# Performance work log

Measured on AMD Instinct MI355X. Metric: run time of the kernel, lower is better.

## Reference

```python
import jax, jax.numpy as jnp
import numpy as np

EC = 256   # ec
CT = 512   # ct
NH = 8     # heads
K = 3      # adaptive pool output
HC = EC // NH
CH = (256, 512, 1024)
HW = (48, 24, 12)
BS = 32
NT = 512   # number of text queries


def _ln(x, g, b, eps=1e-5):
    m = jnp.mean(x, axis=-1, keepdims=True)
    v = jnp.mean((x - m) ** 2, axis=-1, keepdims=True)
    return (x - m) * jax.lax.rsqrt(v + eps) * g + b


def _adaptive_max_pool(x, k):
    # H, W divisible by k -> uniform bins, identical to AdaptiveMaxPool2d
    B, C, H, W = x.shape
    return x.reshape(B, C, k, H // k, k, W // k).max(axis=(3, 5))


def setup_inputs() -> dict:
    key = jax.random.key(0)
    ks = jax.random.split(key, 32)
    d = {}
    for i, (c, s) in enumerate(zip(CH, HW)):
        d[f"x{i}"] = jax.random.normal(ks[i], (BS, c, s, s), jnp.float32)
    d["text"] = jax.random.normal(ks[3], (BS, NT, CT), jnp.float32)
    # 1x1 conv projections (stored as [C_in, EC] matrices)
    for i, c in enumerate(CH):
        d[f"w{i}"] = jax.random.normal(ks[4 + i], (c, EC), jnp.float32) / np.sqrt(c).astype(np.float32)
        d[f"cb{i}"] = jax.random.normal(ks[7 + i], (EC,), jnp.float32) * 0.02
    # LayerNorm + Linear for query (ct->ec), key/value (ec->ec)
    d["q_ln_g"] = jnp.ones((CT,), jnp.float32); d["q_ln_b"] = jnp.zeros((CT,), jnp.float32)
    d["k_ln_g"] = jnp.ones((EC,), jnp.float32); d["k_ln_b"] = jnp.zeros((EC,), jnp.float32)
    d["v_ln_g"] = jnp.ones((EC,), jnp.float32); d["v_ln_b"] = jnp.zeros((EC,), jnp.float32)
    d["q_w"] = jax.random.normal(ks[10], (CT, EC), jnp.float32) / np.sqrt(CT).astype(np.float32)
    d["q_b"] = jax.random.normal(ks[11], (EC,), jnp.float32) * 0.02
    d["k_w"] = jax.random.normal(ks[12], (EC, EC), jnp.float32) / np.sqrt(EC).astype(np.float32)
    d["k_b"] = jax.random.normal(ks[13], (EC,), jnp.float32) * 0.02
    d["v_w"] = jax.random.normal(ks[14], (EC, EC), jnp.float32) / np.sqrt(EC).astype(np.float32)
    d["v_b"] = jax.random.normal(ks[15], (EC,), jnp.float32) * 0.02
    d["proj_w"] = jax.random.normal(ks[16], (EC, CT), jnp.float32) / np.sqrt(EC).astype(np.float32)
    d["proj_b"] = jax.random.normal(ks[17], (CT,), jnp.float32) * 0.02
    return d


def reference(x0, x1, x2, text, w0, cb0, w1, cb1, w2, cb2,
              q_ln_g, q_ln_b, k_ln_g, k_ln_b, v_ln_g, v_ln_b,
              q_w, q_b, k_w, k_b, v_w, v_b, proj_w, proj_b):
    bs = x0.shape[0]
    feats = []
    for x, w, b in ((x0, w0, cb0), (x1, w1, cb1), (x2, w2, cb2)):
        p = jnp.einsum('bchw,ce->behw', x, w) + b[None, :, None, None]  # 1x1 conv
        feats.append(_adaptive_max_pool(p, K).reshape(bs, EC, K * K))
    xc = jnp.concatenate(feats, axis=-1).transpose(0, 2, 1)  # (bs, 27, ec)

    q = _ln(text, q_ln_g, q_ln_b) @ q_w + q_b   # (bs, NT, ec)
    k = _ln(xc, k_ln_g, k_ln_b) @ k_w + k_b     # (bs, 27, ec)
    v = _ln(xc, v_ln_g, v_ln_b) @ v_w + v_b     # (bs, 27, ec)

    q = q.reshape(bs, -1, NH, HC)
    k = k.reshape(bs, -1, NH, HC)
    v = v.reshape(bs, -1, NH, HC)

    aw = jnp.einsum('bnmc,bkmc->bmnk', q, k) / np.sqrt(HC).astype(np.float32)
    aw = jax.nn.softmax(aw, axis=-1)
    o = jnp.einsum('bmnk,bkmc->bnmc', aw, v).reshape(bs, -1, EC)
    return o @ proj_w + proj_b + text  # scale=False -> scale == 1.0
```

## Files before the change

### kernel.cpp

```cpp
#include <hip/hip_runtime.h>
#include <stdint.h>

#define DEVFN __device__ __forceinline__

using f32x4   = __attribute__((ext_vector_type(4)))  float;
using f32x8   = __attribute__((ext_vector_type(8)))  float;
using f32x16  = __attribute__((ext_vector_type(16))) float;
using us4     = __attribute__((ext_vector_type(4)))  unsigned short;
using us8     = __attribute__((ext_vector_type(8)))  unsigned short;
using u32x4   = __attribute__((ext_vector_type(4)))  unsigned int;
using bf16x8  = __attribute__((ext_vector_type(8)))  __bf16;

DEVFN unsigned short f2b(float x){
    union { float f; unsigned u; } v; v.f = x;
    unsigned r = v.u + 0x7FFFu + ((v.u >> 16) & 1u);
    return (unsigned short)(r >> 16);
}
DEVFN float b2f(unsigned short u){
    union { unsigned u; float f; } v; v.u = ((unsigned)u) << 16; return v.f;
}
DEVFN bf16x8 ld_bf16x8(const unsigned short* p){
    return __builtin_bit_cast(bf16x8, *(const us8*)p);
}
DEVFN bf16x8 pack_bf16x8v(f32x8 f){
    us8 u;
#pragma unroll
    for (int j = 0; j < 8; ++j) u[j] = f2b(f[j]);
    return __builtin_bit_cast(bf16x8, u);
}
DEVFN f32x16 zero16(){
    f32x16 z;
#pragma unroll
    for (int i = 0; i < 16; ++i) z[i] = 0.f;
    return z;
}
DEVFN f32x16 mfma_bf16(bf16x8 a, bf16x8 b, f32x16 c){
    return __builtin_amdgcn_mfma_f32_32x32x16_bf16(a, b, c, 0, 0, 0);
}
DEVFN void gload_lds16(const unsigned short* g, unsigned short* l){
    __builtin_amdgcn_global_load_lds(
        (const __attribute__((address_space(1))) unsigned int*)(const void*)g,
        (__attribute__((address_space(3))) unsigned int*)(void*)l,
        16, 0, 0);
}
template<int HW>
DEVFN f32x8 loadA8(const float* ap){
    f32x8 v;
#pragma unroll
    for (int j = 0; j < 8; ++j) v[j] = ap[(size_t)j * HW];
    return v;
}

__global__ __launch_bounds__(256) void k_prep(
        const float* __restrict__ w0, const float* __restrict__ w1,
        const float* __restrict__ w2, const float* __restrict__ qw,
        const float* __restrict__ pw, const float* __restrict__ kw,
        const float* __restrict__ vw,
        unsigned short* __restrict__ o0, unsigned short* __restrict__ o1,
        unsigned short* __restrict__ o2, unsigned short* __restrict__ oq,
        unsigned short* __restrict__ op, unsigned short* __restrict__ ok,
        unsigned short* __restrict__ ov){
    int gid = blockIdx.x * 256 + threadIdx.x;
    const float* in; unsigned short* out; int t, E;
    if (gid < 8192)       { in = w0; out = o0; t = gid;         E = 256; }
    else if (gid < 24576) { in = w1; out = o1; t = gid - 8192;  E = 256; }
    else if (gid < 57344) { in = w2; out = o2; t = gid - 24576; E = 256; }
    else if (gid < 73728) { in = qw; out = oq; t = gid - 57344; E = 256; }
    else if (gid < 90112) { in = pw; out = op; t = gid - 73728; E = 512; }
    else if (gid < 98304) { in = kw; out = ok; t = gid - 90112; E = 256; }
    else                  { in = vw; out = ov; t = gid - 98304; E = 256; }
    int lane = t & 63, fn = t >> 6;
    int nt, ks;
    if (E == 512){ nt = fn & 15; ks = fn >> 4; }
    else         { nt = fn & 7;  ks = fn >> 3; }
    int c0 = ks*16 + (lane >> 5)*8, e = nt*32 + (lane & 31);
    us8 u;
#pragma unroll
    for (int j = 0; j < 8; ++j) u[j] = f2b(in[(size_t)(c0 + j) * E + e]);
    *(us8*)(out + (size_t)t * 8) = u;
}

DEVFN void comp2(f32x16 (&acc)[4], f32x8 a, const unsigned short* bsmr, int kk, int ntb, int lane){
    bf16x8 A = pack_bf16x8v(a);
#pragma unroll
    for (int i = 0; i < 4; ++i){
        bf16x8 B = ld_bf16x8(bsmr + (kk*8 + ntb + i) * 512 + lane * 8);
        acc[i] = mfma_bf16(A, B, acc[i]);
    }
}

template<int C, int WIMG, int BINW>
DEVFN void conv_sub(const float* __restrict__ X, const unsigned short* __restrict__ WF,
                    unsigned short* bsm0, unsigned short* bsm1,
                    int b, int bin, int sub, int ntb, float* rmax){
    const int HW = WIMG * WIMG;
    const int NCH = C / 32;
    int w8 = threadIdx.x >> 6, lane = threadIdx.x & 63, lo = lane & 31, hi = lane >> 5;
    int binr = bin / 3, binc = bin % 3;
    int prow, pcol;
    if constexpr (BINW == 16){ prow = sub*2 + (lo>>4); pcol = lo & 15; }
    else if constexpr (BINW == 8){ prow = sub*4 + (lo>>3); pcol = lo & 7; }
    else { prow = (lo & 15) >> 2; pcol = lo & 3; }
    int gr = binr * BINW + prow, gc = binc * BINW + pcol;
    const float* Xk = X + (size_t)b * C * HW + gr * WIMG + gc + (size_t)hi * 8 * HW;

    f32x16 acc[4];
#pragma unroll
    for (int i = 0; i < 4; ++i) acc[i] = zero16();

    auto stage = [&](unsigned short* dst, int ch){
        const unsigned short* src = WF + (size_t)ch * 8192 + w8 * 1024 + lane * 8;
        unsigned short* dl = dst + w8 * 1024;
        gload_lds16(src,       dl);
        gload_lds16(src + 512, dl + 512);
    };

    __syncthreads();
    stage(bsm0, 0);
    f32x8 a0 = loadA8<HW>(Xk);
    f32x8 a1 = loadA8<HW>(Xk + (size_t)16 * HW);
    __syncthreads();

    unsigned short* cur = bsm0;
    unsigned short* nxt = bsm1;
    for (int c = 0; c < NCH; ++c){
        f32x8 p0, p1;
        bool more = (c + 1 < NCH);
        if (more){
            stage(nxt, c + 1);
            const float* Xn = Xk + (size_t)(c + 1) * 32 * HW;
            p0 = loadA8<HW>(Xn);
            p1 = loadA8<HW>(Xn + (size_t)16 * HW);
        }
        comp2(acc, a0, cur, 0, ntb, lane);
        comp2(acc, a1, cur, 1, ntb, lane);
        __syncthreads();
        if (more){ a0 = p0; a1 = p1; }
        unsigned short* t = cur; cur = nxt; nxt = t;
    }
#pragma unroll
    for (int i = 0; i < 4; ++i){
        float m = acc[i][0];
#pragma unroll
        for (int r = 1; r < 16; ++r) m = fmaxf(m, acc[i][r]);
        rmax[i] = fmaxf(rmax[i], m);
    }
}

__global__ __launch_bounds__(512, 2) void k_convlnq(
        const float* __restrict__ x0, const float* __restrict__ x1, const float* __restrict__ x2,
        const unsigned short* __restrict__ wt0, const unsigned short* __restrict__ wt1,
        const unsigned short* __restrict__ wt2,
        const float* __restrict__ cb0, const float* __restrict__ cb1, const float* __restrict__ cb2,
        float* __restrict__ xc,
        const float* __restrict__ text, const float* __restrict__ qg,
        const float* __restrict__ qbb, const unsigned short* __restrict__ qwt,
        const float* __restrict__ qb, unsigned short* __restrict__ qout){
    __shared__ __attribute__((aligned(16))) char smem[36864];
    unsigned short* bsm0 = (unsigned short*)smem;
    unsigned short* bsm1 = (unsigned short*)(smem + 16384);
    float (*red)[4][32] = (float (*)[4][32])(smem + 32768);
    int blk = blockIdx.x, w = threadIdx.x >> 6, lane = threadIdx.x & 63;
    int lo = lane & 31, hi = lane >> 5;

    if (blk < 544){
        int ntb = (w >> 2) * 4;
        float rmax[4];
#pragma unroll
        for (int i = 0; i < 4; ++i) rmax[i] = -3.4e38f;

        if (blk < 96){
            int b = blk / 3, q = blk % 3;
            int bin = q*4 + (w & 3);
            int bc = bin <= 8 ? bin : 8;
            conv_sub<1024, 12, 4>(x2, wt2, bsm0, bsm1, b, bc, 0, ntb, rmax);
#pragma unroll
            for (int i = 0; i < 4; ++i){
                float m = fmaxf(rmax[i], __shfl_xor(rmax[i], 32));
                if (hi == 0 && bin <= 8){
                    int e = (ntb + i)*32 + lo;
                    xc[((size_t)b*27 + 18 + bin)*256 + e] = m + cb2[e];
                }
            }
        } else if (blk < 256){
            int r = blk - 96, b = r / 5, p = r % 5;
            int binA = 2*p;
            bool hasB = (2*p + 1 <= 8);
            int binB = hasB ? 2*p + 1 : binA;
            int bin = ((w >> 1) & 1) ? binB : binA;
            conv_sub<512, 24, 8>(x1, wt1, bsm0, bsm1, b, bin, w & 1, ntb, rmax);
#pragma unroll
            for (int i = 0; i < 4; ++i){
                float m = fmaxf(rmax[i], __shfl_xor(rmax[i], 32));
                if (hi == 0) red[w][i][lo] = m;
            }
            __syncthreads();
            int t = threadIdx.x;
            int binIdx = t >> 8, e = t & 255;
            int half = e >> 7, ntl = (e >> 5) & 3, l = e & 31;
            int w0 = half*4 + binIdx*2;
            float m = fmaxf(red[w0][ntl][l], red[w0+1][ntl][l]);
            if (binIdx == 0)      xc[((size_t)b*27 + 9 + binA)*256 + e] = m + cb1[e];
            else if (hasB)        xc[((size_t)b*27 + 9 + binB)*256 + e] = m + cb1[e];
        } else {
            int r = blk - 256, b = r / 9, bin = r % 9;
            int s0i = w & 3;
            conv_sub<256, 48, 16>(x0, wt0, bsm0, bsm1, b, bin, s0i,     ntb, rmax);
            conv_sub<256, 48, 16>(x0, wt0, bsm0, bsm1, b, bin, s0i + 4, ntb, rmax);
#pragma unroll
            for (int i = 0; i < 4; ++i){
                float m = fmaxf(rmax[i], __shfl_xor(rmax[i], 32));
                if (hi == 0) red[w][i][lo] = m;
            }
            __syncthreads();
            int t = threadIdx.x;
            if (t < 256){
                int e = t, half = e >> 7, ntl = (e >> 5) & 3, l = e & 31;
                int wb = half * 4;
                float m = fmaxf(fmaxf(red[wb][ntl][l], red[wb+1][ntl][l]),
                                fmaxf(red[wb+2][ntl][l], red[wb+3][ntl][l]));
                xc[((size_t)b*27 + bin)*256 + e] = m + cb0[e];
            }
        }
    } else {
        unsigned short* alds = (unsigned short*)smem;
        size_t row0 = (size_t)(blk - 544) * 32;
        const float* gp = qg  + lane * 8;
        const float* bp = qbb + lane * 8;
        f32x4 g0 = *(const f32x4*)gp, g1 = *(const f32x4*)(gp+4);
        f32x4 b0 = *(const f32x4*)bp, b1 = *(const f32x4*)(bp+4);
#pragma unroll
        for (int it = 0; it < 4; ++it){
            int r = it * 8 + w;
            const float* p = text + (row0 + r) * 512 + lane * 8;
            f32x4 a = *(const f32x4*)p;
            f32x4 c = *(const f32x4*)(p + 4);
            float s = a[0]+a[1]+a[2]+a[3]+c[0]+c[1]+c[2]+c[3];
#pragma unroll
            for (int off = 32; off; off >>= 1) s += __shfl_xor(s, off);
            float mean = s * (1.f/512.f);
            float d[8];
            d[0]=a[0]-mean; d[1]=a[1]-mean; d[2]=a[2]-mean; d[3]=a[3]-mean;
            d[4]=c[0]-mean; d[5]=c[1]-mean; d[6]=c[2]-mean; d[7]=c[3]-mean;
            float vs = d[0]*d[0]+d[1]*d[1]+d[2]*d[2]+d[3]*d[3]+d[4]*d[4]+d[5]*d[5]+d[6]*d[6]+d[7]*d[7];
#pragma unroll
            for (int off = 32; off; off >>= 1) vs += __shfl_xor(vs, off);
            float rstd = rsqrtf(vs * (1.f/512.f) + 1e-5f);
            us8 o;
#pragma unroll
            for (int j = 0; j < 4; ++j) o[j]   = f2b(d[j]  *rstd*g0[j] + b0[j]);
#pragma unroll
            for (int j = 0; j < 4; ++j) o[4+j] = f2b(d[4+j]*rstd*g1[j] + b1[j]);
            *(us8*)(alds + (size_t)r * 520 + lane * 8) = o;
        }
        __syncthreads();

        f32x16 acc = zero16();
        const unsigned short* wf = qwt + (size_t)lane * 8;
        int nt = w;
        for (int ks = 0; ks < 32; ++ks){
            bf16x8 a = ld_bf16x8(alds + (size_t)lo * 520 + ks*16 + hi*8);
            bf16x8 bfr = ld_bf16x8(wf + (size_t)(ks*8 + nt) * 512);
            acc = mfma_bf16(a, bfr, acc);
        }
        int e = nt * 32 + lo;
        float qbias = qb[e];
#pragma unroll
        for (int r = 0; r < 16; ++r){
            size_t row = row0 + (r & 3) + 8 * (r >> 2) + 4 * hi;
            qout[row * 256 + e] = f2b(acc[r] + qbias);
        }
    }
}

__global__ __launch_bounds__(256) void k_kv(const float* __restrict__ xc,
        const float* __restrict__ kg, const float* __restrict__ kb,
        const float* __restrict__ vg, const float* __restrict__ vb,
        const unsigned short* __restrict__ kwt, const unsigned short* __restrict__ vwt,
        const float* __restrict__ k_bias, const float* __restrict__ v_bias,
        float* __restrict__ kout, float* __restrict__ vout){
    __shared__ unsigned short lnk[32][264];
    __shared__ unsigned short lnv[32][264];
    int w = threadIdx.x >> 6, lane = threadIdx.x & 63, lo = lane & 31, hi = lane >> 5;
    size_t row0 = (size_t)blockIdx.x * 32;
    int c0 = lane * 4;
    f32x4 kgv = *(const f32x4*)(kg + c0), kbv = *(const f32x4*)(kb + c0);
    f32x4 vgv = *(const f32x4*)(vg + c0), vbv = *(const f32x4*)(vb + c0);
#pragma unroll
    for (int rr = 0; rr < 8; ++rr){
        int r = w * 8 + rr;
        f32x4 xv = *(const f32x4*)(xc + (row0 + r) * 256 + c0);
        float s = xv[0]+xv[1]+xv[2]+xv[3];
#pragma unroll
        for (int off = 32; off; off >>= 1) s += __shfl_xor(s, off);
        float mean = s * (1.f/256.f);
        float d0 = xv[0]-mean, d1 = xv[1]-mean, d2 = xv[2]-mean, d3 = xv[3]-mean;
        float vs = d0*d0 + d1*d1 + d2*d2 + d3*d3;
#pragma unroll
        for (int off = 32; off; off >>= 1) vs += __shfl_xor(vs, off);
        float rstd = rsqrtf(vs * (1.f/256.f) + 1e-5f);
        us4 uk, uv;
        uk[0] = f2b(d0*rstd*kgv[0] + kbv[0]); uv[0] = f2b(d0*rstd*vgv[0] + vbv[0]);
        uk[1] = f2b(d1*rstd*kgv[1] + kbv[1]); uv[1] = f2b(d1*rstd*vgv[1] + vbv[1]);
        uk[2] = f2b(d2*rstd*kgv[2] + kbv[2]); uv[2] = f2b(d2*rstd*vgv[2] + vbv[2]);
        uk[3] = f2b(d3*rstd*kgv[3] + kbv[3]); uv[3] = f2b(d3*rstd*vgv[3] + vbv[3]);
        *(us4*)(&lnk[r][c0]) = uk;
        *(us4*)(&lnv[r][c0]) = uv;
    }
    __syncthreads();

    f32x16 acc[4];
#pragma unroll
    for (int i = 0; i < 4; ++i) acc[i] = zero16();
    const unsigned short* lds = (w < 2) ? &lnk[0][0] : &lnv[0][0];
    const unsigned short* wf  = ((w < 2) ? kwt : vwt) + (size_t)lane * 8;
    int ntb = (w & 1) * 4;
    for (int ks = 0; ks < 16; ++ks){
        bf16x8 a = ld_bf16x8(lds + lo*264 + ks*16 + hi*8);
#pragma unroll
        for (int i = 0; i < 4; ++i){
            int nt = ntb + i;
            bf16x8 bfr = ld_bf16x8(wf + (size_t)(ks*8 + nt) * 512);
            acc[i] = mfma_bf16(a, bfr, acc[i]);
        }
    }
    const float* bias = (w < 2) ? k_bias : v_bias;
    float* outp = (w < 2) ? kout : vout;
#pragma unroll
    for (int i = 0; i < 4; ++i){
        int e = (ntb + i) * 32 + lo;
        float bv = bias[e];
#pragma unroll
        for (int r = 0; r < 16; ++r){
            size_t row = row0 + (r & 3) + 8 * (r >> 2) + 4 * hi;
            outp[row * 256 + e] = acc[i][r] + bv;
        }
    }
}

__global__ __launch_bounds__(256, 3) void k_attnproj(const unsigned short* __restrict__ qbf,
        const float* __restrict__ kbuf, const float* __restrict__ vbuf,
        const unsigned short* __restrict__ pwt, const float* __restrict__ pb,
        const float* __restrict__ text, float* __restrict__ out){
    int b = blockIdx.x >> 4;
    int rg = blockIdx.x & 15;
    __shared__ unsigned short klds[32][264];
    __shared__ unsigned short vT[256][36];
    __shared__ unsigned short qolds[32][264];
    int tid = threadIdx.x;
    int w = tid >> 6, lane = tid & 63, lo = lane & 31, hi = lane >> 5;
    size_t grow0 = (size_t)b * 512 + rg * 32;

    for (int i = tid; i < 27 * 64; i += 256){
        int row = i >> 6, c4 = (i & 63) << 2;
        f32x4 kv = *(const f32x4*)(kbuf + ((size_t)b*27 + row) * 256 + c4);
        us4 u; u[0]=f2b(kv[0]); u[1]=f2b(kv[1]); u[2]=f2b(kv[2]); u[3]=f2b(kv[3]);
        *(us4*)(&klds[row][c4]) = u;
    }
    for (int i = tid; i < 330; i += 256){
        int row = 27 + i / 66, c4 = (i % 66) * 4;
        us4 z = {0,0,0,0};
        *(us4*)(&klds[row][c4]) = z;
    }
    {
        int ch = tid;
        for (int k = 0; k < 27; ++k)
            vT[ch][k] = f2b(vbuf[((size_t)b*27 + k) * 256 + ch]);
#pragma unroll
        for (int k = 27; k < 36; ++k) vT[ch][k] = 0;
    }
    for (int i = tid; i < 1024; i += 256){
        int row = i >> 5, c8 = (i & 31) << 3;
        *(us8*)(&qolds[row][c8]) = *(const us8*)(qbf + (grow0 + row) * 256 + c8);
    }
    __syncthreads();

#pragma unroll
    for (int hh = 0; hh < 2; ++hh){
        int h = w + hh * 4;
        int hc = h * 32;
        f32x16 s = zero16();
        {
            bf16x8 A0 = ld_bf16x8(&klds[lo][hc + hi*8]);
            bf16x8 B0 = ld_bf16x8(&qolds[lo][hc + hi*8]);
            s = mfma_bf16(A0, B0, s);
            bf16x8 A1 = ld_bf16x8(&klds[lo][hc + 16 + hi*8]);
            bf16x8 B1 = ld_bf16x8(&qolds[lo][hc + 16 + hi*8]);
            s = mfma_bf16(A1, B1, s);
        }
        float mx = -3.4e38f;
#pragma unroll
        for (int r = 0; r < 16; ++r){
            bool valid = hi ? (r < 12) : (r != 15);
            if (valid) mx = fmaxf(mx, s[r]);
        }
        mx = fmaxf(mx, __shfl_xor(mx, 32));
        float p[16]; float sum = 0.f;
#pragma unroll
        for (int r = 0; r < 16; ++r){
            bool valid = hi ? (r < 12) : (r != 15);
            p[r] = valid ? __expf((s[r] - mx) * 0.17677669529663687f) : 0.f;
            sum += p[r];
        }
        sum += __shfl_xor(sum, 32);
        float inv = 1.f / sum;
        unsigned pd[8];
#pragma unroll
        for (int i = 0; i < 8; ++i)
            pd[i] = (unsigned)f2b(p[2*i]*inv) | ((unsigned)f2b(p[2*i+1]*inv) << 16);

        f32x16 o = zero16();
#pragma unroll
        for (int c = 0; c < 2; ++c){
            unsigned own0 = hi ? pd[4*c+2] : pd[4*c];
            unsigned own1 = hi ? pd[4*c+3] : pd[4*c+1];
            unsigned snd0 = hi ? pd[4*c]   : pd[4*c+2];
            unsigned snd1 = hi ? pd[4*c+1] : pd[4*c+3];
            unsigned rcv0 = (unsigned)__shfl_xor((int)snd0, 32);
            unsigned rcv1 = (unsigned)__shfl_xor((int)snd1, 32);
            u32x4 bd;
            bd[0] = hi ? rcv0 : own0;
            bd[1] = hi ? rcv1 : own1;
            bd[2] = hi ? own0 : rcv0;
            bd[3] = hi ? own1 : rcv1;
            bf16x8 B = __builtin_bit_cast(bf16x8, bd);
            bf16x8 A = ld_bf16x8(&vT[hc + lo][c*16 + hi*8]);
            o = mfma_bf16(A, B, o);
        }
#pragma unroll
        for (int g = 0; g < 4; ++g){
            us4 u;
#pragma unroll
            for (int j = 0; j < 4; ++j) u[j] = f2b(o[g*4 + j]);
            *(us4*)(&qolds[lo][hc + g*8 + hi*4]) = u;
        }
    }
    __syncthreads();

    f32x16 acc[4];
#pragma unroll
    for (int i = 0; i < 4; ++i) acc[i] = zero16();
    const unsigned short* wf = pwt + (size_t)lane * 8;
    for (int ks = 0; ks < 16; ++ks){
        bf16x8 a = ld_bf16x8(&qolds[lo][ks*16 + hi*8]);
#pragma unroll
        for (int i = 0; i < 4; ++i){
            int nt = w*4 + i;
            bf16x8 bfr = ld_bf16x8(wf + (size_t)(ks*16 + nt) * 512);
            acc[i] = mfma_bf16(a, bfr, acc[i]);
        }
    }
#pragma unroll
    for (int i = 0; i < 4; ++i){
        int ct = (w*4 + i) * 32 + lo;
        float pbias = pb[ct];
#pragma unroll
        for (int r = 0; r < 16; ++r){
            size_t row = grow0 + (r & 3) + 8 * (r >> 2) + 4 * hi;
            out[row * 512 + ct] = acc[i][r] + pbias + text[row * 512 + ct];
        }
    }
}

extern "C" void kernel_launch(void* const* d_in, const int* in_sizes, int n_in,
                              void* d_out, int out_size, void* d_ws, size_t ws_size,
                              hipStream_t stream) {
    (void)in_sizes; (void)n_in; (void)out_size; (void)ws_size;
    const float* x0     = (const float*)d_in[0];
    const float* x1     = (const float*)d_in[1];
    const float* x2     = (const float*)d_in[2];
    const float* text   = (const float*)d_in[3];
    const float* w0     = (const float*)d_in[4];
    const float* cb0    = (const float*)d_in[5];
    const float* w1     = (const float*)d_in[6];
    const float* cb1    = (const float*)d_in[7];
    const float* w2     = (const float*)d_in[8];
    const float* cb2    = (const float*)d_in[9];
    const float* q_ln_g = (const float*)d_in[10];
    const float* q_ln_b = (const float*)d_in[11];
    const float* k_ln_g = (const float*)d_in[12];
    const float* k_ln_b = (const float*)d_in[13];
    const float* v_ln_g = (const float*)d_in[14];
    const float* v_ln_b = (const float*)d_in[15];
    const float* q_w    = (const float*)d_in[16];
    const float* q_b    = (const float*)d_in[17];
    const float* k_w    = (const float*)d_in[18];
    const float* k_b    = (const float*)d_in[19];
    const float* v_w    = (const float*)d_in[20];
    const float* v_b    = (const float*)d_in[21];
    const float* proj_w = (const float*)d_in[22];
    const float* proj_b = (const float*)d_in[23];
    float* out = (float*)d_out;

    char* wsb = (char*)d_ws; size_t off = 0;
    auto take = [&](size_t bytes) -> void* {
        void* p = wsb + off; off += (bytes + 255) & ~(size_t)255; return p;
    };
    unsigned short* qbf    = (unsigned short*)take((size_t)16384 * 256 * 2);
    float*          xc     = (float*)take((size_t)32 * 27 * 256 * 4);
    float*          kbuf   = (float*)take((size_t)32 * 27 * 256 * 4);
    float*          vbuf   = (float*)take((size_t)32 * 27 * 256 * 4);
    unsigned short* wt0    = (unsigned short*)take((size_t)256 * 256 * 2);
    unsigned short* wt1    = (unsigned short*)take((size_t)256 * 512 * 2);
    unsigned short* wt2    = (unsigned short*)take((size_t)256 * 1024 * 2);
    unsigned short* qwt    = (unsigned short*)take((size_t)256 * 512 * 2);
    unsigned short* pwt    = (unsigned short*)take((size_t)512 * 256 * 2);
    unsigned short* kwt    = (unsigned short*)take((size_t)256 * 256 * 2);
    unsigned short* vwt    = (unsigned short*)take((size_t)256 * 256 * 2);

    k_prep<<<416, 256, 0, stream>>>(w0, w1, w2, q_w, proj_w, k_w, v_w,
                                    wt0, wt1, wt2, qwt, pwt, kwt, vwt);
    k_convlnq<<<1056, 512, 0, stream>>>(x0, x1, x2, wt0, wt1, wt2, cb0, cb1, cb2, xc,
                                        text, q_ln_g, q_ln_b, qwt, q_b, qbf);
    k_kv<<<27, 256, 0, stream>>>(xc, k_ln_g, k_ln_b, v_ln_g, v_ln_b,
                                 kwt, vwt, k_b, v_b, kbuf, vbuf);
    k_attnproj<<<512, 256, 0, stream>>>(qbf, kbuf, vbuf, pwt, proj_b, text, out);
}
```

Before: 120.9 us.

## Deepen conv weight staging to a 4-slot LDS ring with explicit vmcnt waits

```diff
diff --git a/kernel.cpp b/kernel.cpp
--- a/kernel.cpp
+++ b/kernel.cpp
@@ -91,7 +91,7 @@
 
 template<int C, int WIMG, int BINW>
 DEVFN void conv_sub(const float* __restrict__ X, const unsigned short* __restrict__ WF,
-                    unsigned short* bsm0, unsigned short* bsm1,
+                    unsigned short* bsm,
                     int b, int bin, int sub, int ntb, float* rmax){
     const int HW = WIMG * WIMG;
     const int NCH = C / 32;
@@ -108,35 +108,39 @@
 #pragma unroll
     for (int i = 0; i < 4; ++i) acc[i] = zero16();
 
-    auto stage = [&](unsigned short* dst, int ch){
-        const unsigned short* src = WF + (size_t)ch * 8192 + w8 * 1024 + lane * 8;
-        unsigned short* dl = dst + w8 * 1024;
+    auto stage = [&](int ci){
+        const unsigned short* src = WF + (size_t)ci * 8192 + w8 * 1024 + lane * 8;
+        unsigned short* dl = bsm + (size_t)(ci & 3) * 8192 + w8 * 1024;
         gload_lds16(src,       dl);
         gload_lds16(src + 512, dl + 512);
     };
 
     __syncthreads();
-    stage(bsm0, 0);
+    stage(0);
     f32x8 a0 = loadA8<HW>(Xk);
     f32x8 a1 = loadA8<HW>(Xk + (size_t)16 * HW);
-    __syncthreads();
-
-    unsigned short* cur = bsm0;
-    unsigned short* nxt = bsm1;
-    for (int c = 0; c < NCH; ++c){
-        f32x8 p0, p1;
-        bool more = (c + 1 < NCH);
+    stage(1);
+
+    for (int i = 0; i < NCH; ++i){
+        if (i + 2 < NCH) stage(i + 2);
+        __builtin_amdgcn_sched_barrier(0);
+        f32x8 n0, n1;
+        bool more = (i + 1 < NCH);
         if (more){
-            stage(nxt, c + 1);
-            const float* Xn = Xk + (size_t)(c + 1) * 32 * HW;
-            p0 = loadA8<HW>(Xn);
-            p1 = loadA8<HW>(Xn + (size_t)16 * HW);
-        }
+            const float* Xn = Xk + (size_t)(i + 1) * 32 * HW;
+            n0 = loadA8<HW>(Xn);
+            n1 = loadA8<HW>(Xn + (size_t)16 * HW);
+        }
+        __builtin_amdgcn_sched_barrier(0);
+        if (i < NCH - 1) asm volatile("s_waitcnt vmcnt(36)" ::: "memory");
+        else             asm volatile("s_waitcnt vmcnt(32)" ::: "memory");
+        __builtin_amdgcn_sched_barrier(0);
+        __builtin_amdgcn_s_barrier();
+        __builtin_amdgcn_sched_barrier(0);
+        const unsigned short* cur = bsm + (size_t)(i & 3) * 8192;
         comp2(acc, a0, cur, 0, ntb, lane);
         comp2(acc, a1, cur, 1, ntb, lane);
-        __syncthreads();
-        if (more){ a0 = p0; a1 = p1; }
-        unsigned short* t = cur; cur = nxt; nxt = t;
+        if (more){ a0 = n0; a1 = n1; }
     }
 #pragma unroll
     for (int i = 0; i < 4; ++i){
@@ -156,10 +160,9 @@
         const float* __restrict__ text, const float* __restrict__ qg,
         const float* __restrict__ qbb, const unsigned short* __restrict__ qwt,
         const float* __restrict__ qb, unsigned short* __restrict__ qout){
-    __shared__ __attribute__((aligned(16))) char smem[36864];
-    unsigned short* bsm0 = (unsigned short*)smem;
-    unsigned short* bsm1 = (unsigned short*)(smem + 16384);
-    float (*red)[4][32] = (float (*)[4][32])(smem + 32768);
+    __shared__ __attribute__((aligned(16))) char smem[69632];
+    unsigned short* bsm = (unsigned short*)smem;
+    float (*red)[4][32] = (float (*)[4][32])(smem + 65536);
     int blk = blockIdx.x, w = threadIdx.x >> 6, lane = threadIdx.x & 63;
     int lo = lane & 31, hi = lane >> 5;
 
@@ -173,7 +176,7 @@
             int b = blk / 3, q = blk % 3;
             int bin = q*4 + (w & 3);
             int bc = bin <= 8 ? bin : 8;
-            conv_sub<1024, 12, 4>(x2, wt2, bsm0, bsm1, b, bc, 0, ntb, rmax);
+            conv_sub<1024, 12, 4>(x2, wt2, bsm, b, bc, 0, ntb, rmax);
 #pragma unroll
             for (int i = 0; i < 4; ++i){
                 float m = fmaxf(rmax[i], __shfl_xor(rmax[i], 32));
@@ -188,7 +191,7 @@
             bool hasB = (2*p + 1 <= 8);
             int binB = hasB ? 2*p + 1 : binA;
             int bin = ((w >> 1) & 1) ? binB : binA;
-            conv_sub<512, 24, 8>(x1, wt1, bsm0, bsm1, b, bin, w & 1, ntb, rmax);
+            conv_sub<512, 24, 8>(x1, wt1, bsm, b, bin, w & 1, ntb, rmax);
 #pragma unroll
             for (int i = 0; i < 4; ++i){
                 float m = fmaxf(rmax[i], __shfl_xor(rmax[i], 32));
@@ -205,8 +208,8 @@
         } else {
             int r = blk - 256, b = r / 9, bin = r % 9;
             int s0i = w & 3;
-            conv_sub<256, 48, 16>(x0, wt0, bsm0, bsm1, b, bin, s0i,     ntb, rmax);
-            conv_sub<256, 48, 16>(x0, wt0, bsm0, bsm1, b, bin, s0i + 4, ntb, rmax);
+            conv_sub<256, 48, 16>(x0, wt0, bsm, b, bin, s0i,     ntb, rmax);
+            conv_sub<256, 48, 16>(x0, wt0, bsm, b, bin, s0i + 4, ntb, rmax);
 #pragma unroll
             for (int i = 0; i < 4; ++i){
                 float m = fmaxf(rmax[i], __shfl_xor(rmax[i], 32));
```

After: 152.1 us. +25.7%, slower.
